# Kernel tuning notes

Hardware: AMD Instinct MI355X
Metric: run time of the kernel (lower is better)

The kernel has to match this reference:

```python
import jax, jax.numpy as jnp
import numpy as np

BATCH = 512          # bs_large + bs_small
COMBINED_BS = 320    # bs_large + bs_small // (r_large // r_small)
R = 64               # r_large
K = 4096             # hidden dim, fixed in the TIR kernel
N_ADAPT = 80         # combined adapters


def setup_inputs() -> dict:
    key = jax.random.key(0)
    k1, k2, k3, k4 = jax.random.split(key, 4)
    x = jax.random.normal(k1, (BATCH, 1, K), dtype=jnp.float32)
    xids = jax.random.randint(k2, (COMBINED_BS * R,), 0, BATCH, dtype=jnp.int32)
    wids = jax.random.randint(k3, (COMBINED_BS,), 0, N_ADAPT, dtype=jnp.int32)
    A = jax.random.normal(k4, (N_ADAPT, K, R), dtype=jnp.float32) * 0.02
    return {"x": x, "xids": xids, "wids": wids, "A": A}


def reference(x, xids, wids, A):
    # out[c, 0, r] = sum_k x[xids[c*R + r], 0, k] * A[wids[c], k, r]
    C = wids.shape[0]
    r = A.shape[2]
    tok = xids.reshape(C, r)          # per-output-element token ids
    xg = x[tok, 0, :]                 # (C, R, K) gathered activations
    Ag = A[wids]                      # (C, K, R) gathered adapters
    out = jnp.einsum('crk,ckr->cr', xg, Ag)
    return out[:, None, :]            # (C, 1, R)
```

## Files before the change

kernel.cpp:

```cpp
#include <hip/hip_runtime.h>
#include <stdint.h>

namespace {
constexpr int BATCH  = 512;
constexpr int CBS    = 320;
constexpr int R      = 64;
constexpr int K      = 4096;
constexpr int NADAPT = 80;
constexpr int SPLIT  = 8;
constexpr int KS     = K / SPLIT;
constexpr int TK     = 64;
constexpr int NT     = 256;
constexpr int NW     = NT / 64;
constexpr int NTILES = KS / TK;

constexpr size_t WS_X_OFF  = 4096;
constexpr size_t WS_NEEDED = WS_X_OFF + (size_t)BATCH * K * 2;

__device__ inline uint16_t f2bf(float f) {
    uint32_t u = __float_as_uint(f);
    u += 0x7fffu + ((u >> 16) & 1u);
    return (uint16_t)(u >> 16);
}
__device__ inline float bf2f(uint16_t b) {
    return __uint_as_float((uint32_t)b << 16);
}
}

__global__ void sort_by_wid(const int* __restrict__ wids, int* __restrict__ perm)
{
    __shared__ int hist[NADAPT];
    __shared__ int offs[NADAPT];
    const int t = threadIdx.x;
    if (t < NADAPT) hist[t] = 0;
    __syncthreads();
    atomicAdd(&hist[wids[t]], 1);
    __syncthreads();
    if (t == 0) {
        int run = 0;
        for (int i = 0; i < NADAPT; ++i) { offs[i] = run; run += hist[i]; }
    }
    __syncthreads();
    const int pos = atomicAdd(&offs[wids[t]], 1);
    perm[pos] = t;
}

__global__ __launch_bounds__(256)
void cvt_x(const float* __restrict__ x, uint16_t* __restrict__ xb)
{
    const int i = blockIdx.x * 256 + threadIdx.x;
    const float4 v = ((const float4*)x)[i];
    ushort4 o;
    o.x = f2bf(v.x); o.y = f2bf(v.y); o.z = f2bf(v.z); o.w = f2bf(v.w);
    ((ushort4*)xb)[i] = o;
}

__global__ __launch_bounds__(NT)
void lora_main(const int* __restrict__ xids,
               const int* __restrict__ wids,
               const float* __restrict__ A,
               const uint16_t* __restrict__ xb,
               const int* __restrict__ perm,
               float* __restrict__ out)
{
    __shared__ float xs[TK * R];
    __shared__ float red[NW * R];

    const int bid  = blockIdx.x;
    const int i0   = bid >> 3;
    const int s    = bid & 7;
    const int c    = perm[i0];
    const int t    = threadIdx.x;
    const int wave = t >> 6;
    const int lane = t & 63;
    const int r4   = lane & 15;
    const int kq   = lane >> 4;

    const int wid = wids[c];
    const float* __restrict__ Aw = A + (size_t)wid * (K * R);

    const int rw  = t >> 2;
    const int jq  = t & 3;
    const int tok = xids[c * R + rw];
    const uint16_t* __restrict__ xrow = xb + (size_t)tok * K + s * KS + jq * 16;
    const int rsw = rw ^ (jq * 16);

    float4 acc = make_float4(0.f, 0.f, 0.f, 0.f);

    uint4 p0, p1;
    {
        const uint4* src = (const uint4*)xrow;
        p0 = src[0]; p1 = src[1];
    }

    for (int tile = 0; tile < NTILES; ++tile) {
        {
            const uint32_t w[8] = {p0.x, p0.y, p0.z, p0.w, p1.x, p1.y, p1.z, p1.w};
            float* base = xs + (jq * 16) * R + rsw;
#pragma unroll
            for (int m = 0; m < 8; ++m) {
                base[(2 * m + 0) * R] = bf2f((uint16_t)(w[m] & 0xffffu));
                base[(2 * m + 1) * R] = bf2f((uint16_t)(w[m] >> 16));
            }
        }
        __syncthreads();

        if (tile + 1 < NTILES) {
            const uint4* src = (const uint4*)(xrow + (tile + 1) * TK);
            p0 = src[0]; p1 = src[1];
        }

        const int kw = wave * 16 + kq;
        const int rr = (4 * r4) ^ (wave * 16);
        const float* __restrict__ Ap =
            Aw + (size_t)(s * KS + tile * TK + kw) * R + 4 * r4;
#pragma unroll
        for (int i = 0; i < 4; ++i) {
            float4 av = *(const float4*)(Ap + (size_t)(4 * i) * R);
            float4 xv = *(const float4*)(&xs[(kw + 4 * i) * R + rr]);
            acc.x = fmaf(xv.x, av.x, acc.x);
            acc.y = fmaf(xv.y, av.y, acc.y);
            acc.z = fmaf(xv.z, av.z, acc.z);
            acc.w = fmaf(xv.w, av.w, acc.w);
        }
        __syncthreads();
    }

#pragma unroll
    for (int m = 16; m < 64; m <<= 1) {
        acc.x += __shfl_xor(acc.x, m, 64);
        acc.y += __shfl_xor(acc.y, m, 64);
        acc.z += __shfl_xor(acc.z, m, 64);
        acc.w += __shfl_xor(acc.w, m, 64);
    }
    if (kq == 0) {
        float* rd = &red[wave * R + 4 * r4];
        rd[0] = acc.x; rd[1] = acc.y; rd[2] = acc.z; rd[3] = acc.w;
    }
    __syncthreads();
    if (wave == 0) {
        float sum = red[lane] + red[R + lane] + red[2 * R + lane] + red[3 * R + lane];
        atomicAdd(&out[c * R + lane], sum);
    }
}

__global__ __launch_bounds__(NT)
void lora_fallback(const float* __restrict__ x,
                   const int*   __restrict__ xids,
                   const int*   __restrict__ wids,
                   const float* __restrict__ A,
                   float*       __restrict__ out)
{
    __shared__ float xs[TK * R];
    __shared__ float red[NW * R];
    const int bid  = blockIdx.x;
    const int c    = bid >> 3;
    const int s    = bid & 7;
    const int t    = threadIdx.x;
    const int wave = t >> 6;
    const int lane = t & 63;
    const int r4   = lane & 15;
    const int kq   = lane >> 4;
    const int wid  = wids[c];
    const float* __restrict__ Aw = A + (size_t)wid * (K * R);
    const int rw  = t >> 2;
    const int jq  = t & 3;
    const int tok = xids[c * R + rw];
    const float* __restrict__ xrow = x + (size_t)tok * K + s * KS + jq * 16;
    float4 acc = make_float4(0.f, 0.f, 0.f, 0.f);
    float4 pv[4];
    {
        const float4* src = (const float4*)xrow;
#pragma unroll
        for (int ii = 0; ii < 4; ++ii) pv[ii] = src[ii];
    }
    for (int tile = 0; tile < NTILES; ++tile) {
#pragma unroll
        for (int ii = 0; ii < 4; ++ii) {
            const int kk = jq * 16 + ii * 4;
            xs[(kk + 0) * R + rw] = pv[ii].x;
            xs[(kk + 1) * R + rw] = pv[ii].y;
            xs[(kk + 2) * R + rw] = pv[ii].z;
            xs[(kk + 3) * R + rw] = pv[ii].w;
        }
        __syncthreads();
        if (tile + 1 < NTILES) {
            const float4* src = (const float4*)(xrow + (tile + 1) * TK);
#pragma unroll
            for (int ii = 0; ii < 4; ++ii) pv[ii] = src[ii];
        }
        const int kw = wave * 16 + kq;
        const float* __restrict__ Ap =
            Aw + (size_t)(s * KS + tile * TK + kw) * R + 4 * r4;
#pragma unroll
        for (int i = 0; i < 4; ++i) {
            float4 av = *(const float4*)(Ap + (size_t)(4 * i) * R);
            float4 xv = *(const float4*)(&xs[(kw + 4 * i) * R + 4 * r4]);
            acc.x = fmaf(xv.x, av.x, acc.x);
            acc.y = fmaf(xv.y, av.y, acc.y);
            acc.z = fmaf(xv.z, av.z, acc.z);
            acc.w = fmaf(xv.w, av.w, acc.w);
        }
        __syncthreads();
    }
#pragma unroll
    for (int m = 16; m < 64; m <<= 1) {
        acc.x += __shfl_xor(acc.x, m, 64);
        acc.y += __shfl_xor(acc.y, m, 64);
        acc.z += __shfl_xor(acc.z, m, 64);
        acc.w += __shfl_xor(acc.w, m, 64);
    }
    if (kq == 0) {
        float* rd = &red[wave * R + 4 * r4];
        rd[0] = acc.x; rd[1] = acc.y; rd[2] = acc.z; rd[3] = acc.w;
    }
    __syncthreads();
    if (wave == 0) {
        float sum = red[lane] + red[R + lane] + red[2 * R + lane] + red[3 * R + lane];
        atomicAdd(&out[c * R + lane], sum);
    }
}

extern "C" void kernel_launch(void* const* d_in, const int* in_sizes, int n_in,
                              void* d_out, int out_size, void* d_ws, size_t ws_size,
                              hipStream_t stream)
{
    (void)in_sizes; (void)n_in;
    const float* x    = (const float*)d_in[0];
    const int*   xids = (const int*)d_in[1];
    const int*   wids = (const int*)d_in[2];
    const float* A    = (const float*)d_in[3];
    float* out        = (float*)d_out;

    hipMemsetAsync(out, 0, (size_t)out_size * sizeof(float), stream);

    if (ws_size >= WS_NEEDED) {
        int*      perm = (int*)d_ws;
        uint16_t* xb   = (uint16_t*)((char*)d_ws + WS_X_OFF);
        hipLaunchKernelGGL(sort_by_wid, dim3(1), dim3(CBS), 0, stream, wids, perm);
        hipLaunchKernelGGL(cvt_x, dim3(BATCH * K / 4 / 256), dim3(256), 0, stream, x, xb);
        hipLaunchKernelGGL(lora_main, dim3(CBS * SPLIT), dim3(NT), 0, stream,
                           xids, wids, A, xb, perm, out);
    } else {
        hipLaunchKernelGGL(lora_fallback, dim3(CBS * SPLIT), dim3(NT), 0, stream,
                           x, xids, wids, A, out);
    }
}
```

Measured before the change: 146.9 us.

## Fuse prep kernels and keep bf16 activations packed in double-buffered LDS

Merges the wid sort, the fp32-to-bf16 conversion of x and the output zeroing into one prep kernel, replacing three launches plus a memset with a single launch. The main kernel now stores x as packed bf16 pairs in a double-buffered, XOR-swizzled shared tile and unpacks them only at the FMA. This halves LDS traffic and allows one barrier per tile instead of two. It adds a launch-bounds occupancy hint and a changed thread-to-row mapping with narrower 8-byte gathers, which may affect global load coalescing.

```diff
diff --git a/kernel.cpp b/kernel.cpp
--- a/kernel.cpp
+++ b/kernel.cpp
@@ -25,37 +25,51 @@
 __device__ inline float bf2f(uint16_t b) {
     return __uint_as_float((uint32_t)b << 16);
 }
-}
-
-__global__ void sort_by_wid(const int* __restrict__ wids, int* __restrict__ perm)
-{
-    __shared__ int hist[NADAPT];
-    __shared__ int offs[NADAPT];
-    const int t = threadIdx.x;
-    if (t < NADAPT) hist[t] = 0;
-    __syncthreads();
-    atomicAdd(&hist[wids[t]], 1);
-    __syncthreads();
-    if (t == 0) {
-        int run = 0;
-        for (int i = 0; i < NADAPT; ++i) { offs[i] = run; run += hist[i]; }
-    }
-    __syncthreads();
-    const int pos = atomicAdd(&offs[wids[t]], 1);
-    perm[pos] = t;
+__device__ inline float bflo(uint32_t u) { return __uint_as_float(u << 16); }
+__device__ inline float bfhi(uint32_t u) { return __uint_as_float(u & 0xffff0000u); }
 }
 
 __global__ __launch_bounds__(256)
-void cvt_x(const float* __restrict__ x, uint16_t* __restrict__ xb)
-{
-    const int i = blockIdx.x * 256 + threadIdx.x;
-    const float4 v = ((const float4*)x)[i];
-    ushort4 o;
-    o.x = f2bf(v.x); o.y = f2bf(v.y); o.z = f2bf(v.z); o.w = f2bf(v.w);
-    ((ushort4*)xb)[i] = o;
-}
-
-__global__ __launch_bounds__(NT)
+void prep(const float* __restrict__ x, uint16_t* __restrict__ xb,
+          const int* __restrict__ wids, int* __restrict__ perm,
+          float* __restrict__ out, int out_size)
+{
+    const int bid = blockIdx.x;
+    const int t   = threadIdx.x;
+    if (bid == 0) {
+        __shared__ int hist[NADAPT];
+        __shared__ int offs[NADAPT];
+        if (t < NADAPT) hist[t] = 0;
+        __syncthreads();
+        for (int c = t; c < CBS; c += 256) atomicAdd(&hist[wids[c]], 1);
+        __syncthreads();
+        if (t == 0) {
+            int run = 0;
+            for (int i = 0; i < NADAPT; ++i) { offs[i] = run; run += hist[i]; }
+        }
+        __syncthreads();
+        for (int c = t; c < CBS; c += 256) {
+            const int pos = atomicAdd(&offs[wids[c]], 1);
+            perm[pos] = c;
+        }
+    } else if (bid <= BATCH * K / 1024) {
+        const int i = (bid - 1) * 256 + t;
+        const float4 v = ((const float4*)x)[i];
+        ushort4 o;
+        o.x = f2bf(v.x); o.y = f2bf(v.y); o.z = f2bf(v.z); o.w = f2bf(v.w);
+        ((ushort4*)xb)[i] = o;
+    } else {
+        const int i4 = (bid - (1 + BATCH * K / 1024)) * 256 + t;
+        const int e  = i4 * 4;
+        if (e + 3 < out_size) {
+            ((float4*)out)[i4] = make_float4(0.f, 0.f, 0.f, 0.f);
+        } else {
+            for (int q = e; q < out_size; ++q) out[q] = 0.f;
+        }
+    }
+}
+
+__global__ __launch_bounds__(NT, 8)
 void lora_main(const int* __restrict__ xids,
                const int* __restrict__ wids,
                const float* __restrict__ A,
@@ -63,7 +77,7 @@
                const int* __restrict__ perm,
                float* __restrict__ out)
 {
-    __shared__ float xs[TK * R];
+    __shared__ uint32_t xs[2][(TK / 2) * R];
     __shared__ float red[NW * R];
 
     const int bid  = blockIdx.x;
@@ -71,7 +85,7 @@
     const int s    = bid & 7;
     const int c    = perm[i0];
     const int t    = threadIdx.x;
-    const int wave = t >> 6;
+    const int wv   = t >> 6;
     const int lane = t & 63;
     const int r4   = lane & 15;
     const int kq   = lane >> 4;
@@ -79,51 +93,69 @@
     const int wid = wids[c];
     const float* __restrict__ Aw = A + (size_t)wid * (K * R);
 
-    const int rw  = t >> 2;
-    const int jq  = t & 3;
-    const int tok = xids[c * R + rw];
-    const uint16_t* __restrict__ xrow = xb + (size_t)tok * K + s * KS + jq * 16;
-    const int rsw = rw ^ (jq * 16);
+    const int kc = t & 15;
+    const int rg = t >> 4;
+    uint32_t rowoff[4];
+#pragma unroll
+    for (int j = 0; j < 4; ++j)
+        rowoff[j] = (uint32_t)xids[c * R + 4 * rg + j] * K;
+    const uint16_t* __restrict__ xbase = xb + (size_t)s * KS + kc * 4;
+    const int colw = (4 * rg) ^ (kc << 2);
+    const int w0i  = (2 * kc + 0) * R + colw;
+    const int w1i  = (2 * kc + 1) * R + colw;
+
+    const size_t aBase = (size_t)(s * KS + 16 * wv + 2 * kq) * R + 4 * r4;
 
     float4 acc = make_float4(0.f, 0.f, 0.f, 0.f);
 
-    uint4 p0, p1;
     {
-        const uint4* src = (const uint4*)xrow;
-        p0 = src[0]; p1 = src[1];
-    }
-
+        uint2 L0 = *(const uint2*)(xbase + rowoff[0]);
+        uint2 L1 = *(const uint2*)(xbase + rowoff[1]);
+        uint2 L2 = *(const uint2*)(xbase + rowoff[2]);
+        uint2 L3 = *(const uint2*)(xbase + rowoff[3]);
+        *(uint4*)&xs[0][w0i] = make_uint4(L0.x, L1.x, L2.x, L3.x);
+        *(uint4*)&xs[0][w1i] = make_uint4(L0.y, L1.y, L2.y, L3.y);
+    }
+
+    uint2 P0, P1, P2, P3;
     for (int tile = 0; tile < NTILES; ++tile) {
+        const int nt = tile + 1;
+        if (nt < NTILES) {
+            const uint16_t* src = xbase + nt * TK;
+            P0 = *(const uint2*)(src + rowoff[0]);
+            P1 = *(const uint2*)(src + rowoff[1]);
+            P2 = *(const uint2*)(src + rowoff[2]);
+            P3 = *(const uint2*)(src + rowoff[3]);
+        }
+        __syncthreads();
+
         {
-            const uint32_t w[8] = {p0.x, p0.y, p0.z, p0.w, p1.x, p1.y, p1.z, p1.w};
-            float* base = xs + (jq * 16) * R + rsw;
-#pragma unroll
-            for (int m = 0; m < 8; ++m) {
-                base[(2 * m + 0) * R] = bf2f((uint16_t)(w[m] & 0xffffu));
-                base[(2 * m + 1) * R] = bf2f((uint16_t)(w[m] >> 16));
+            const uint32_t* __restrict__ B = xs[tile & 1];
+            const float* __restrict__ At = Aw + aBase + (size_t)tile * TK * R;
+#pragma unroll
+            for (int i = 0; i < 2; ++i) {
+                const int k2  = wv * 8 + kq + 4 * i;
+                const int col = (4 * r4) ^ (((k2 >> 1) & 15) << 2);
+                const uint4 xv = *(const uint4*)&B[k2 * R + col];
+                const float* Ap = At + (size_t)(8 * i) * R;
+                const float4 a0 = *(const float4*)Ap;
+                const float4 a1 = *(const float4*)(Ap + R);
+                acc.x = fmaf(bflo(xv.x), a0.x, acc.x);
+                acc.x = fmaf(bfhi(xv.x), a1.x, acc.x);
+                acc.y = fmaf(bflo(xv.y), a0.y, acc.y);
+                acc.y = fmaf(bfhi(xv.y), a1.y, acc.y);
+                acc.z = fmaf(bflo(xv.z), a0.z, acc.z);
+                acc.z = fmaf(bfhi(xv.z), a1.z, acc.z);
+                acc.w = fmaf(bflo(xv.w), a0.w, acc.w);
+                acc.w = fmaf(bfhi(xv.w), a1.w, acc.w);
             }
         }
-        __syncthreads();
-
-        if (tile + 1 < NTILES) {
-            const uint4* src = (const uint4*)(xrow + (tile + 1) * TK);
-            p0 = src[0]; p1 = src[1];
-        }
-
-        const int kw = wave * 16 + kq;
-        const int rr = (4 * r4) ^ (wave * 16);
-        const float* __restrict__ Ap =
-            Aw + (size_t)(s * KS + tile * TK + kw) * R + 4 * r4;
-#pragma unroll
-        for (int i = 0; i < 4; ++i) {
-            float4 av = *(const float4*)(Ap + (size_t)(4 * i) * R);
-            float4 xv = *(const float4*)(&xs[(kw + 4 * i) * R + rr]);
-            acc.x = fmaf(xv.x, av.x, acc.x);
-            acc.y = fmaf(xv.y, av.y, acc.y);
-            acc.z = fmaf(xv.z, av.z, acc.z);
-            acc.w = fmaf(xv.w, av.w, acc.w);
-        }
-        __syncthreads();
+
+        if (nt < NTILES) {
+            const int b = nt & 1;
+            *(uint4*)&xs[b][w0i] = make_uint4(P0.x, P1.x, P2.x, P3.x);
+            *(uint4*)&xs[b][w1i] = make_uint4(P0.y, P1.y, P2.y, P3.y);
+        }
     }
 
 #pragma unroll
@@ -133,12 +165,13 @@
         acc.z += __shfl_xor(acc.z, m, 64);
         acc.w += __shfl_xor(acc.w, m, 64);
     }
+    __syncthreads();
     if (kq == 0) {
-        float* rd = &red[wave * R + 4 * r4];
+        float* rd = &red[wv * R + 4 * r4];
         rd[0] = acc.x; rd[1] = acc.y; rd[2] = acc.z; rd[3] = acc.w;
     }
     __syncthreads();
-    if (wave == 0) {
+    if (wv == 0) {
         float sum = red[lane] + red[R + lane] + red[2 * R + lane] + red[3 * R + lane];
         atomicAdd(&out[c * R + lane], sum);
     }
@@ -151,7 +184,7 @@
                    const float* __restrict__ A,
                    float*       __restrict__ out)
 {
-    __shared__ float xs[TK * R];
+    __shared__ float xsf[TK * R];
     __shared__ float red[NW * R];
     const int bid  = blockIdx.x;
     const int c    = bid >> 3;
@@ -178,10 +211,10 @@
 #pragma unroll
         for (int ii = 0; ii < 4; ++ii) {
             const int kk = jq * 16 + ii * 4;
-            xs[(kk + 0) * R + rw] = pv[ii].x;
-            xs[(kk + 1) * R + rw] = pv[ii].y;
-            xs[(kk + 2) * R + rw] = pv[ii].z;
-            xs[(kk + 3) * R + rw] = pv[ii].w;
+            xsf[(kk + 0) * R + rw] = pv[ii].x;
+            xsf[(kk + 1) * R + rw] = pv[ii].y;
+            xsf[(kk + 2) * R + rw] = pv[ii].z;
+            xsf[(kk + 3) * R + rw] = pv[ii].w;
         }
         __syncthreads();
         if (tile + 1 < NTILES) {
@@ -195,7 +228,7 @@
 #pragma unroll
         for (int i = 0; i < 4; ++i) {
             float4 av = *(const float4*)(Ap + (size_t)(4 * i) * R);
-            float4 xv = *(const float4*)(&xs[(kw + 4 * i) * R + 4 * r4]);
+            float4 xv = *(const float4*)(&xsf[(kw + 4 * i) * R + 4 * r4]);
             acc.x = fmaf(xv.x, av.x, acc.x);
             acc.y = fmaf(xv.y, av.y, acc.y);
             acc.z = fmaf(xv.z, av.z, acc.z);
@@ -232,16 +265,17 @@
     const float* A    = (const float*)d_in[3];
     float* out        = (float*)d_out;
 
-    hipMemsetAsync(out, 0, (size_t)out_size * sizeof(float), stream);
-
     if (ws_size >= WS_NEEDED) {
         int*      perm = (int*)d_ws;
-        uint16_t* xb   = (uint16_t*)((char*)d_ws + WS_X_OFF);
-        hipLaunchKernelGGL(sort_by_wid, dim3(1), dim3(CBS), 0, stream, wids, perm);
-        hipLaunchKernelGGL(cvt_x, dim3(BATCH * K / 4 / 256), dim3(256), 0, stream, x, xb);
+        uint16_t* xbw  = (uint16_t*)((char*)d_ws + WS_X_OFF);
+        const int ncvt = BATCH * K / 1024;
+        const int nz   = (out_size + 1023) / 1024;
+        hipLaunchKernelGGL(prep, dim3(1 + ncvt + nz), dim3(256), 0, stream,
+                           x, xbw, wids, perm, out, out_size);
         hipLaunchKernelGGL(lora_main, dim3(CBS * SPLIT), dim3(NT), 0, stream,
-                           xids, wids, A, xb, perm, out);
+                           xids, wids, A, xbw, perm, out);
     } else {
+        hipMemsetAsync(out, 0, (size_t)out_size * sizeof(float), stream);
         hipLaunchKernelGGL(lora_fallback, dim3(CBS * SPLIT), dim3(NT), 0, stream,
                            x, xids, wids, A, out);
     }
```

Measured after the change: 149.2 us. No clear change (+1.6%).
